# Kernel optimization log

Hardware: AMD Instinct MI355X
Metric: run time of the kernel (lower is better)

The kernel has to match this reference:

```python
import jax, jax.numpy as jnp
import numpy as np

EPS = 1e-08
F_DIM = 512


def setup_inputs() -> dict:
    key = jax.random.key(0)
    ks = jax.random.split(key, 7)
    N, F = 50000, F_DIM
    q = jax.random.normal(ks[0], (N, 1, F), dtype=jnp.float32)
    mu = jax.random.normal(ks[1], (N, 3, F), dtype=jnp.float32)
    # Xavier-ish scaled params
    W_mix = jax.random.normal(ks[2], (2 * F, F), dtype=jnp.float32) * (1.0 / np.sqrt(F))
    W1 = jax.random.normal(ks[3], (F, 2 * F), dtype=jnp.float32) * (1.0 / np.sqrt(2 * F))
    b1 = jnp.zeros((F,), dtype=jnp.float32)
    W2 = jax.random.normal(ks[4], (3 * F, F), dtype=jnp.float32) * (1.0 / np.sqrt(F))
    b2 = jnp.zeros((3 * F,), dtype=jnp.float32)
    return {"q": q, "mu": mu, "W_mix": W_mix, "W1": W1, "b1": b1, "W2": W2, "b2": b2}


def reference(q, mu, W_mix, W1, b1, W2, b2):
    F = q.shape[-1]
    # mu_channel_mix: [N,3,F] @ [F,2F] -> [N,3,2F]
    mu_mix = jnp.einsum('ndf,gf->ndg', mu, W_mix)
    mu_V, mu_W = mu_mix[..., :F], mu_mix[..., F:]
    # vector norm over Cartesian axis -> [N,1,F]
    mu_Vn = jnp.sqrt(jnp.sum(mu_V * mu_V, axis=-2, keepdims=True) + EPS)
    ctx = jnp.concatenate([q, mu_Vn], axis=-1)  # [N,1,2F]
    h = jax.nn.silu(jnp.einsum('nsf,gf->nsg', ctx, W1) + b1)  # [N,1,F]
    x = jnp.einsum('nsf,gf->nsg', h, W2) + b2  # [N,1,3F]
    dq_intra = x[..., :F]
    dmu_intra = x[..., F:2 * F] * mu_W  # broadcast [N,1,F]*[N,3,F]
    dqmu_intra = x[..., 2 * F:] * jnp.sum(mu_V * mu_W, axis=1, keepdims=True)
    q_out = q + dq_intra + dqmu_intra
    mu_out = mu + dmu_intra
    return (q_out, mu_out)
```

## Files before the change

kernel.cpp:

```cpp
#include <hip/hip_runtime.h>
#include <stdint.h>

#define NN 50000
#define QWORDS 25600000

typedef __attribute__((ext_vector_type(8))) short bf16x8;
typedef __attribute__((ext_vector_type(4))) float f32x4;

__device__ __forceinline__ uint32_t f2bf(float x){
  uint32_t u = __builtin_bit_cast(uint32_t, x);
  u += 0x7FFFu + ((u >> 16) & 1u);
  return u >> 16;
}
__device__ __forceinline__ float bf2f(uint32_t b){
  uint32_t u = b << 16;
  return __builtin_bit_cast(float, u);
}
__device__ __forceinline__ void gload16(const uint16_t* g, uint16_t* l){
  __builtin_amdgcn_global_load_lds(
      (const __attribute__((address_space(1))) uint32_t*)g,
      (__attribute__((address_space(3))) uint32_t*)l, 16, 0, 0);
}
__device__ __forceinline__ f32x4 mfma16(bf16x8 a, bf16x8 b, f32x4 c){
  return __builtin_amdgcn_mfma_f32_16x16x32_bf16(a, b, c, 0, 0, 0);
}

#define FENCE() asm volatile("" ::: "memory")

__global__ void k_convert(const float* __restrict__ wmix, const float* __restrict__ w1,
                          const float* __restrict__ w2, uint16_t* __restrict__ dst){
  int i = blockIdx.x * 256 + threadIdx.x;
  int e = i << 2;
  const float* s; int o;
  if (e < 524288)       { s = wmix; o = e; }
  else if (e < 1048576) { s = w1;   o = e - 524288; }
  else                  { s = w2;   o = e - 1048576; }
  f32x4 v = *(const f32x4*)(s + o);
  uint2 pk;
  pk.x = f2bf(v[0]) | (f2bf(v[1]) << 16);
  pk.y = f2bf(v[2]) | (f2bf(v[3]) << 16);
  *(uint2*)(dst + e) = pk;
}

__global__ __launch_bounds__(512, 4)
void k_gemm1(const float* __restrict__ mu, const uint16_t* __restrict__ wmixb,
             uint16_t* __restrict__ qh, float* __restrict__ muW){
  __shared__ uint16_t As[2][12288];
  __shared__ uint16_t Bs[2][8192];
  const int tid  = threadIdx.x;
  const int lane = tid & 63;
  const int w    = tid >> 6;
  const int wn   = w & 3;
  const int wf   = w >> 2;
  const int orig = blockIdx.x;
  const int j    = (orig & 7) * 782 + (orig >> 3);
  const int f0   = (j & 7) * 64;
  const int n0   = (j >> 3) * 64;
  const int lrow = tid >> 4;
  const int lcol = (tid & 15) * 4;

  f32x4 ar[6];
  auto A_LOAD = [&](int ks){
    const int k0 = ks * 64;
    #pragma unroll
    for (int p=0; p<6; ++p){
      int r = p*32 + lrow;
      int d = r >> 6, nrow = r & 63;
      int n = n0 + nrow;
      int g = (n < NN ? n : NN-1)*3 + d;
      ar[p] = *(const f32x4*)(mu + (size_t)g*512 + k0 + lcol);
    }
  };
  auto A_WRITE = [&](int buf){
    #pragma unroll
    for (int p=0; p<6; ++p){
      int r = p*32 + lrow;
      f32x4 v = ar[p];
      uint2 pk;
      pk.x = f2bf(v[0]) | (f2bf(v[1]) << 16);
      pk.y = f2bf(v[2]) | (f2bf(v[3]) << 16);
      *(uint2*)&As[buf][r*64 + (lcol ^ ((r&7)<<3))] = pk;
    }
  };
  auto B_ISSUE = [&](int ks, int buf){
    const int k0 = ks * 64;
    #pragma unroll
    for (int jj=0; jj<2; ++jj){
      int jb = w*2 + jj;
      int row = jb*8 + (lane>>3);
      int g = (row < 64) ? (f0 + row) : (448 + f0 + row);
      int srcc = ((lane&7) ^ ((lane>>3)&7)) * 8;
      gload16(wmixb + (size_t)g*512 + k0 + srcc, &Bs[buf][jb*512]);
    }
  };

  const f32x4 z4 = {0.f,0.f,0.f,0.f};
  f32x4 acc[3][4];
  #pragma unroll
  for (int d=0; d<3; ++d)
    #pragma unroll
    for (int nt=0; nt<4; ++nt) acc[d][nt] = z4;

  A_LOAD(0); B_ISSUE(0, 0); A_WRITE(0);
  for (int ks=0; ks<8; ++ks){
    const int cur = ks & 1;
    __syncthreads();
    if (ks < 7){ A_LOAD(ks+1); B_ISSUE(ks+1, cur^1); }
    #pragma unroll
    for (int kf=0; kf<2; ++kf){
      int kc = kf*32 + (lane>>4)*8;
      bf16x8 af[3];
      #pragma unroll
      for (int d=0; d<3; ++d){
        int r = d*64 + wn*16 + (lane&15);
        af[d] = *(const bf16x8*)&As[cur][r*64 + (kc ^ ((r&7)<<3))];
      }
      #pragma unroll
      for (int nt=0; nt<4; ++nt){
        int ntg = wf*2 + (nt&1) + (nt>>1)*4;
        int rr = ntg*16 + (lane&15);
        bf16x8 bf = *(const bf16x8*)&Bs[cur][rr*64 + (kc ^ ((rr&7)<<3))];
        #pragma unroll
        for (int d=0; d<3; ++d)
          acc[d][nt] = mfma16(af[d], bf, acc[d][nt]);
      }
    }
    if (ks < 7) A_WRITE(cur^1);
  }

  const int rb4 = (lane >> 4) * 4;
  #pragma unroll
  for (int c=0; c<2; ++c){
    #pragma unroll
    for (int jx=0; jx<4; ++jx){
      int n = n0 + wn*16 + rb4 + jx;
      if (n >= NN) continue;
      int f = f0 + (wf*2 + c)*16 + (lane & 15);
      float v0 = acc[0][c][jx],   v1 = acc[1][c][jx],   v2 = acc[2][c][jx];
      float u0 = acc[0][c+2][jx], u1 = acc[1][c+2][jx], u2 = acc[2][c+2][jx];
      float vn = sqrtf(v0*v0 + v1*v1 + v2*v2 + 1e-8f);
      float dt = v0*u0 + v1*u1 + v2*u2;
      qh[(size_t)n*1024 + f]       = (uint16_t)f2bf(vn);
      qh[(size_t)n*1024 + 512 + f] = (uint16_t)f2bf(dt);
      size_t mb = (size_t)n*1536 + f;
      muW[mb] = u0; muW[mb+512] = u1; muW[mb+1024] = u2;
    }
  }
}

__global__ __launch_bounds__(256, 2)
void k_gemm2(const float* __restrict__ q, const uint16_t* __restrict__ w1b,
             const float* __restrict__ b1, uint16_t* __restrict__ qh){
  __shared__ uint16_t A2[2][2048];
  __shared__ uint16_t B2[2][16384];
  const int tid  = threadIdx.x;
  const int lane = tid & 63;
  const int w    = tid >> 6;
  const int wm   = w >> 1;
  const int wn   = w & 1;
  const int n0   = blockIdx.x * 64;

  f32x4 qa0, qa1;
  auto QA_LOAD = [&](int s){
    int k0 = s*32;
    int row = tid >> 2, ch = tid & 3;
    int nc = (n0 + row < NN) ? n0 + row : NN-1;
    qa0 = *(const f32x4*)(q + (size_t)nc*512 + k0 + ch*8);
    qa1 = *(const f32x4*)(q + (size_t)nc*512 + k0 + ch*8 + 4);
  };
  auto QA_WRITE = [&](int buf){
    int row = tid >> 2, ch = tid & 3;
    uint4 pk;
    pk.x = f2bf(qa0[0]) | (f2bf(qa0[1]) << 16);
    pk.y = f2bf(qa0[2]) | (f2bf(qa0[3]) << 16);
    pk.z = f2bf(qa1[0]) | (f2bf(qa1[1]) << 16);
    pk.w = f2bf(qa1[2]) | (f2bf(qa1[3]) << 16);
    *(uint4*)&A2[buf][row*32 + ((ch ^ (row&3)))*8] = pk;
  };
  auto VA_ISSUE = [&](int s, int buf){
    int k0v = (s-16)*32;
    int row = w*16 + (lane>>2);
    int nc = (n0 + row < NN) ? n0 + row : NN-1;
    int srcch = (lane&3) ^ (row&3);
    gload16(qh + (size_t)nc*1024 + k0v + srcch*8, &A2[buf][w*512]);
  };
  auto B_ISSUE = [&](int s, int buf){
    int k0 = s*32;
    #pragma unroll
    for (int jj=0; jj<8; ++jj){
      int j = w*8 + jj;
      int row = j*16 + (lane>>2);
      int srcch = (lane&3) ^ (row&3);
      gload16(w1b + (size_t)row*1024 + k0 + srcch*8, &B2[buf][j*512]);
    }
  };

  const f32x4 z4 = {0.f,0.f,0.f,0.f};
  f32x4 acc2[2][16];
  #pragma unroll
  for (int mt=0; mt<2; ++mt)
    #pragma unroll
    for (int nt=0; nt<16; ++nt) acc2[mt][nt] = z4;

  QA_LOAD(0); B_ISSUE(0, 0); QA_WRITE(0);
  for (int s=0; s<32; ++s){
    const int cur = s & 1;
    __syncthreads();
    if (s < 31){
      if (s+1 < 16) QA_LOAD(s+1); else VA_ISSUE(s+1, cur^1);
      B_ISSUE(s+1, cur^1);
    }
    {
      int kc = (lane>>4)*8;
      bf16x8 a[2];
      #pragma unroll
      for (int mt=0; mt<2; ++mt){
        int r = wm*32 + mt*16 + (lane&15);
        a[mt] = *(const bf16x8*)&A2[cur][r*32 + (kc ^ ((r&3)<<3))];
      }
      #pragma unroll
      for (int nt=0; nt<16; ++nt){
        int rr = wn*256 + nt*16 + (lane&15);
        bf16x8 b = *(const bf16x8*)&B2[cur][rr*32 + (kc ^ ((rr&3)<<3))];
        acc2[0][nt] = mfma16(a[0], b, acc2[0][nt]);
        acc2[1][nt] = mfma16(a[1], b, acc2[1][nt]);
      }
    }
    if (s < 31 && s+1 < 16) QA_WRITE(cur^1);
  }

  const int rb4 = (lane >> 4) * 4;
  #pragma unroll
  for (int nt=0; nt<16; ++nt){
    int col = wn*256 + nt*16 + (lane&15);
    float bb = b1[col];
    #pragma unroll
    for (int mt=0; mt<2; ++mt)
      #pragma unroll
      for (int j=0; j<4; ++j){
        int n = n0 + wm*32 + mt*16 + rb4 + j;
        if (n < NN){
          float x = acc2[mt][nt][j] + bb;
          float sv = x / (1.f + __expf(-x));
          qh[(size_t)n*1024 + col] = (uint16_t)f2bf(sv);
        }
      }
  }
}

__global__ __launch_bounds__(512, 4)
void k_gemm3(const float* __restrict__ q, const float* __restrict__ mu,
             const uint16_t* __restrict__ w2b, const float* __restrict__ b2,
             float* __restrict__ dout){
  __shared__ uint16_t Hs[32*512];
  __shared__ uint16_t B3[2][12288];
  const int tid  = threadIdx.x;
  const int lane = tid & 63;
  const int w    = tid >> 6;
  const int wm   = w >> 2;
  const int wn   = w & 3;
  const int n0   = blockIdx.x * 32;
  const uint16_t* qh = (const uint16_t*)dout;
  float* mout = dout + (size_t)QWORDS;
  const int l15 = lane & 15;
  const int rb4 = (lane >> 4) * 4;
  const f32x4 z4 = {0.f,0.f,0.f,0.f};

  #pragma unroll
  for (int i=0; i<4; ++i){
    int row = w*4 + i;
    int nc = (n0 + row < NN) ? n0 + row : NN-1;
    gload16(qh + (size_t)nc*1024 + (size_t)((lane ^ (row&7))*8), &Hs[row*512]);
  }

  auto B_ISSUE = [&](int it, int ks, uint16_t* slot){
    #pragma unroll
    for (int jj=0; jj<3; ++jj){
      int j = w*3 + jj;
      int rr = j*8 + (lane>>3);
      int s3 = rr >> 6, fi = rr & 63;
      int g = s3*512 + it*64 + fi;
      gload16(w2b + (size_t)g*512 + ks*64 + ((lane&7) ^ (rr&7))*8, slot + j*512);
    }
  };
  B_ISSUE(0, 0, B3[0]);

  float dtv[4], qv[4], muv[3][4], mwv[3][4];
  float bb0=0.f, bb1=0.f, bb2=0.f;
  int   fq = 0;
  f32x4 acc3[3];

#define K3_MFMA(KS) do{ \
    const uint16_t* bsl = B3[(KS)&1]; \
    __builtin_amdgcn_s_setprio(1); \
    _Pragma("unroll") \
    for (int kf=0; kf<2; ++kf){ \
      int r = wm*16 + l15; \
      int ch = ((KS)*8 + kf*4 + (lane>>4)) ^ (r&7); \
      bf16x8 a = *(const bf16x8*)&Hs[r*512 + ch*8]; \
      _Pragma("unroll") \
      for (int s3=0; s3<3; ++s3){ \
        int rr = s3*64 + wn*16 + l15; \
        int chb = (kf*4 + (lane>>4)) ^ (rr&7); \
        bf16x8 b = *(const bf16x8*)&bsl[rr*64 + chb*8]; \
        acc3[s3] = mfma16(a, b, acc3[s3]); \
      } \
    } \
    __builtin_amdgcn_s_setprio(0); \
  } while(0)

  #pragma unroll 1
  for (int it=0; it<8; ++it){
    if (it) { asm volatile("s_waitcnt vmcnt(16)" ::: "memory"); }
    else    { asm volatile("s_waitcnt vmcnt(0)"  ::: "memory"); }
    __builtin_amdgcn_s_barrier();
    B_ISSUE(it, 1, B3[1]);
    FENCE();
    {
      #pragma unroll
      for (int s3=0; s3<3; ++s3) acc3[s3] = z4;
      fq = it*64 + wn*16 + l15;
      bb0 = b2[fq]; bb1 = b2[512+fq]; bb2 = b2[1024+fq];
      #pragma unroll
      for (int p=0; p<4; ++p){
        int n = n0 + wm*16 + rb4 + p;
        int nc = n < NN ? n : NN-1;
        dtv[p] = bf2f(qh[(size_t)nc*1024 + 512 + fq]);
        qv[p]  = q[(size_t)nc*512 + fq];
      }
    }
    FENCE();
    K3_MFMA(0);

    asm volatile("s_waitcnt vmcnt(11)" ::: "memory");
    __builtin_amdgcn_s_barrier();
    B_ISSUE(it, 2, B3[0]);
    FENCE();
    {
      #pragma unroll
      for (int p=0; p<4; ++p){
        int n = n0 + wm*16 + rb4 + p;
        int nc = n < NN ? n : NN-1;
        size_t mb = (size_t)nc*1536 + fq;
        muv[0][p] = mu[mb]; muv[1][p] = mu[mb+512]; muv[2][p] = mu[mb+1024];
      }
    }
    FENCE();
    K3_MFMA(1);

    asm volatile("s_waitcnt vmcnt(12)" ::: "memory");
    __builtin_amdgcn_s_barrier();
    B_ISSUE(it, 3, B3[1]);
    FENCE();
    {
      #pragma unroll
      for (int p=0; p<4; ++p){
        int n = n0 + wm*16 + rb4 + p;
        int nc = n < NN ? n : NN-1;
        size_t mb = (size_t)nc*1536 + fq;
        mwv[0][p] = mout[mb]; mwv[1][p] = mout[mb+512]; mwv[2][p] = mout[mb+1024];
      }
    }
    FENCE();
    K3_MFMA(2);

    asm volatile("s_waitcnt vmcnt(12)" ::: "memory");
    __builtin_amdgcn_s_barrier();
    B_ISSUE(it, 4, B3[0]);
    FENCE();
    K3_MFMA(3);

    asm volatile("s_waitcnt vmcnt(0)" ::: "memory");
    __builtin_amdgcn_s_barrier();
    B_ISSUE(it, 5, B3[1]);
    FENCE();
    K3_MFMA(4);

    asm volatile("s_waitcnt vmcnt(0)" ::: "memory");
    __builtin_amdgcn_s_barrier();
    B_ISSUE(it, 6, B3[0]);
    FENCE();
    K3_MFMA(5);

    asm volatile("s_waitcnt vmcnt(0)" ::: "memory");
    __builtin_amdgcn_s_barrier();
    B_ISSUE(it, 7, B3[1]);
    FENCE();
    K3_MFMA(6);

    asm volatile("s_waitcnt vmcnt(0)" ::: "memory");
    __builtin_amdgcn_s_barrier();
    if (it < 7) B_ISSUE(it+1, 0, B3[0]);
    FENCE();
    K3_MFMA(7);
    {
      #pragma unroll
      for (int p=0; p<4; ++p){
        int n = n0 + wm*16 + rb4 + p;
        if (n < NN){
          float x0 = acc3[0][p] + bb0;
          float x1 = acc3[1][p] + bb1;
          float x2 = acc3[2][p] + bb2;
          dout[(size_t)n*512 + fq] = qv[p] + x0 + x2*dtv[p];
          size_t mb = (size_t)n*1536 + fq;
          mout[mb]      = muv[0][p] + x1*mwv[0][p];
          mout[mb+512]  = muv[1][p] + x1*mwv[1][p];
          mout[mb+1024] = muv[2][p] + x1*mwv[2][p];
        }
      }
    }
  }
#undef K3_MFMA
}

extern "C" void kernel_launch(void* const* d_in, const int* in_sizes, int n_in,
                              void* d_out, int out_size, void* d_ws, size_t ws_size,
                              hipStream_t stream){
  (void)in_sizes; (void)n_in; (void)out_size; (void)ws_size;
  const float* q    = (const float*)d_in[0];
  const float* mu   = (const float*)d_in[1];
  const float* wmix = (const float*)d_in[2];
  const float* w1   = (const float*)d_in[3];
  const float* b1   = (const float*)d_in[4];
  const float* w2   = (const float*)d_in[5];
  const float* b2   = (const float*)d_in[6];
  uint16_t* wb = (uint16_t*)d_ws;
  float* dout = (float*)d_out;

  hipLaunchKernelGGL(k_convert, dim3(1792), dim3(256), 0, stream, wmix, w1, w2, wb);
  hipLaunchKernelGGL(k_gemm1, dim3(6256), dim3(512), 0, stream,
                     mu, wb, (uint16_t*)d_out, dout + (size_t)QWORDS);
  hipLaunchKernelGGL(k_gemm2, dim3(782), dim3(256), 0, stream,
                     q, wb + 524288, b1, (uint16_t*)d_out);
  hipLaunchKernelGGL(k_gemm3, dim3(1563), dim3(512), 0, stream,
                     q, mu, wb + 1048576, b2, dout);
}
```

Measured before the change: 895.2 us.

## Load W2 fragments directly into registers and stage full hidden row in LDS

New measurement: 1.361 ms. 52.0% more time.

```diff
diff --git a/kernel.cpp b/kernel.cpp
--- a/kernel.cpp
+++ b/kernel.cpp
@@ -24,8 +24,6 @@
 __device__ __forceinline__ f32x4 mfma16(bf16x8 a, bf16x8 b, f32x4 c){
   return __builtin_amdgcn_mfma_f32_16x16x32_bf16(a, b, c, 0, 0, 0);
 }
-
-#define FENCE() asm volatile("" ::: "memory")
 
 __global__ void k_convert(const float* __restrict__ wmix, const float* __restrict__ w1,
                           const float* __restrict__ w2, uint16_t* __restrict__ dst){
@@ -252,8 +250,7 @@
 void k_gemm3(const float* __restrict__ q, const float* __restrict__ mu,
              const uint16_t* __restrict__ w2b, const float* __restrict__ b2,
              float* __restrict__ dout){
-  __shared__ uint16_t Hs[32*512];
-  __shared__ uint16_t B3[2][12288];
+  __shared__ uint16_t Hs[32*1024];
   const int tid  = threadIdx.x;
   const int lane = tid & 63;
   const int w    = tid >> 6;
@@ -264,153 +261,86 @@
   float* mout = dout + (size_t)QWORDS;
   const int l15 = lane & 15;
   const int rb4 = (lane >> 4) * 4;
-  const f32x4 z4 = {0.f,0.f,0.f,0.f};
+  const int kof = (lane >> 4) * 8;
 
   #pragma unroll
   for (int i=0; i<4; ++i){
     int row = w*4 + i;
     int nc = (n0 + row < NN) ? n0 + row : NN-1;
-    gload16(qh + (size_t)nc*1024 + (size_t)((lane ^ (row&7))*8), &Hs[row*512]);
-  }
-
-  auto B_ISSUE = [&](int it, int ks, uint16_t* slot){
-    #pragma unroll
-    for (int jj=0; jj<3; ++jj){
-      int j = w*3 + jj;
-      int rr = j*8 + (lane>>3);
-      int s3 = rr >> 6, fi = rr & 63;
-      int g = s3*512 + it*64 + fi;
-      gload16(w2b + (size_t)g*512 + ks*64 + ((lane&7) ^ (rr&7))*8, slot + j*512);
-    }
-  };
-  B_ISSUE(0, 0, B3[0]);
-
-  float dtv[4], qv[4], muv[3][4], mwv[3][4];
-  float bb0=0.f, bb1=0.f, bb2=0.f;
-  int   fq = 0;
-  f32x4 acc3[3];
-
-#define K3_MFMA(KS) do{ \
-    const uint16_t* bsl = B3[(KS)&1]; \
-    __builtin_amdgcn_s_setprio(1); \
-    _Pragma("unroll") \
-    for (int kf=0; kf<2; ++kf){ \
-      int r = wm*16 + l15; \
-      int ch = ((KS)*8 + kf*4 + (lane>>4)) ^ (r&7); \
-      bf16x8 a = *(const bf16x8*)&Hs[r*512 + ch*8]; \
-      _Pragma("unroll") \
-      for (int s3=0; s3<3; ++s3){ \
-        int rr = s3*64 + wn*16 + l15; \
-        int chb = (kf*4 + (lane>>4)) ^ (rr&7); \
-        bf16x8 b = *(const bf16x8*)&bsl[rr*64 + chb*8]; \
-        acc3[s3] = mfma16(a, b, acc3[s3]); \
-      } \
-    } \
-    __builtin_amdgcn_s_setprio(0); \
-  } while(0)
+    int sc = (lane ^ (row&7)) * 8;
+    gload16(qh + (size_t)nc*1024 + sc,       &Hs[row*1024]);
+    gload16(qh + (size_t)nc*1024 + 512 + sc, &Hs[row*1024 + 512]);
+  }
+  asm volatile("s_waitcnt vmcnt(0)" ::: "memory");
+  __syncthreads();
+
+  int nidx[4], rowp[4];
+  #pragma unroll
+  for (int p=0; p<4; ++p){
+    int rr = wm*16 + rb4 + p;
+    rowp[p] = rr;
+    int n = n0 + rr;
+    nidx[p] = n < NN ? n : NN-1;
+  }
 
   #pragma unroll 1
   for (int it=0; it<8; ++it){
-    if (it) { asm volatile("s_waitcnt vmcnt(16)" ::: "memory"); }
-    else    { asm volatile("s_waitcnt vmcnt(0)"  ::: "memory"); }
-    __builtin_amdgcn_s_barrier();
-    B_ISSUE(it, 1, B3[1]);
-    FENCE();
-    {
-      #pragma unroll
-      for (int s3=0; s3<3; ++s3) acc3[s3] = z4;
-      fq = it*64 + wn*16 + l15;
-      bb0 = b2[fq]; bb1 = b2[512+fq]; bb2 = b2[1024+fq];
-      #pragma unroll
-      for (int p=0; p<4; ++p){
-        int n = n0 + wm*16 + rb4 + p;
-        int nc = n < NN ? n : NN-1;
-        dtv[p] = bf2f(qh[(size_t)nc*1024 + 512 + fq]);
-        qv[p]  = q[(size_t)nc*512 + fq];
-      }
-    }
-    FENCE();
-    K3_MFMA(0);
-
-    asm volatile("s_waitcnt vmcnt(11)" ::: "memory");
-    __builtin_amdgcn_s_barrier();
-    B_ISSUE(it, 2, B3[0]);
-    FENCE();
-    {
-      #pragma unroll
-      for (int p=0; p<4; ++p){
-        int n = n0 + wm*16 + rb4 + p;
-        int nc = n < NN ? n : NN-1;
-        size_t mb = (size_t)nc*1536 + fq;
-        muv[0][p] = mu[mb]; muv[1][p] = mu[mb+512]; muv[2][p] = mu[mb+1024];
-      }
-    }
-    FENCE();
-    K3_MFMA(1);
-
-    asm volatile("s_waitcnt vmcnt(12)" ::: "memory");
-    __builtin_amdgcn_s_barrier();
-    B_ISSUE(it, 3, B3[1]);
-    FENCE();
-    {
-      #pragma unroll
-      for (int p=0; p<4; ++p){
-        int n = n0 + wm*16 + rb4 + p;
-        int nc = n < NN ? n : NN-1;
-        size_t mb = (size_t)nc*1536 + fq;
-        mwv[0][p] = mout[mb]; mwv[1][p] = mout[mb+512]; mwv[2][p] = mout[mb+1024];
-      }
-    }
-    FENCE();
-    K3_MFMA(2);
-
-    asm volatile("s_waitcnt vmcnt(12)" ::: "memory");
-    __builtin_amdgcn_s_barrier();
-    B_ISSUE(it, 4, B3[0]);
-    FENCE();
-    K3_MFMA(3);
-
-    asm volatile("s_waitcnt vmcnt(0)" ::: "memory");
-    __builtin_amdgcn_s_barrier();
-    B_ISSUE(it, 5, B3[1]);
-    FENCE();
-    K3_MFMA(4);
-
-    asm volatile("s_waitcnt vmcnt(0)" ::: "memory");
-    __builtin_amdgcn_s_barrier();
-    B_ISSUE(it, 6, B3[0]);
-    FENCE();
-    K3_MFMA(5);
-
-    asm volatile("s_waitcnt vmcnt(0)" ::: "memory");
-    __builtin_amdgcn_s_barrier();
-    B_ISSUE(it, 7, B3[1]);
-    FENCE();
-    K3_MFMA(6);
-
-    asm volatile("s_waitcnt vmcnt(0)" ::: "memory");
-    __builtin_amdgcn_s_barrier();
-    if (it < 7) B_ISSUE(it+1, 0, B3[0]);
-    FENCE();
-    K3_MFMA(7);
-    {
-      #pragma unroll
-      for (int p=0; p<4; ++p){
-        int n = n0 + wm*16 + rb4 + p;
-        if (n < NN){
-          float x0 = acc3[0][p] + bb0;
-          float x1 = acc3[1][p] + bb1;
-          float x2 = acc3[2][p] + bb2;
-          dout[(size_t)n*512 + fq] = qv[p] + x0 + x2*dtv[p];
-          size_t mb = (size_t)n*1536 + fq;
-          mout[mb]      = muv[0][p] + x1*mwv[0][p];
-          mout[mb+512]  = muv[1][p] + x1*mwv[1][p];
-          mout[mb+1024] = muv[2][p] + x1*mwv[2][p];
-        }
-      }
-    }
-  }
-#undef K3_MFMA
+    const int fq = it*64 + wn*16 + l15;
+    const float bb0 = b2[fq], bb1 = b2[512+fq], bb2 = b2[1024+fq];
+    float qv[4], dtv[4], muv[3][4], mwv[3][4];
+    const int dc = fq >> 3, dо = fq & 7;
+    #pragma unroll
+    for (int p=0; p<4; ++p){
+      dtv[p] = bf2f(Hs[rowp[p]*1024 + 512 + ((dc ^ (rowp[p]&7))*8) + dо]);
+      qv[p]  = q[(size_t)nidx[p]*512 + fq];
+      size_t mb = (size_t)nidx[p]*1536 + fq;
+      muv[0][p] = mu[mb];   muv[1][p] = mu[mb+512];   muv[2][p] = mu[mb+1024];
+      mwv[0][p] = mout[mb]; mwv[1][p] = mout[mb+512]; mwv[2][p] = mout[mb+1024];
+    }
+
+    f32x4 acc0 = {0.f,0.f,0.f,0.f}, acc1 = acc0, acc2 = acc0;
+    const uint16_t* bp0 = w2b + (size_t)(it*64 + wn*16 + l15)*512;
+    bf16x8 bc[6], bn[6];
+    auto LDB = [&](bf16x8* dst, int ks){
+      const int ko = ks*64 + kof;
+      #pragma unroll
+      for (int s3=0; s3<3; ++s3){
+        const uint16_t* bp = bp0 + (size_t)s3*512*512;
+        dst[s3*2+0] = *(const bf16x8*)(bp + ko);
+        dst[s3*2+1] = *(const bf16x8*)(bp + ko + 32);
+      }
+    };
+    LDB(bc, 0);
+    #pragma unroll
+    for (int ks=0; ks<8; ++ks){
+      if (ks < 7) LDB(bn, ks+1);
+      const int r = wm*16 + l15;
+      const int ch0 = (ks*8 + 0 + (lane>>4)) ^ (r&7);
+      const int ch1 = (ks*8 + 4 + (lane>>4)) ^ (r&7);
+      bf16x8 a0 = *(const bf16x8*)&Hs[r*1024 + ch0*8];
+      bf16x8 a1 = *(const bf16x8*)&Hs[r*1024 + ch1*8];
+      acc0 = mfma16(a0, bc[0], acc0); acc0 = mfma16(a1, bc[1], acc0);
+      acc1 = mfma16(a0, bc[2], acc1); acc1 = mfma16(a1, bc[3], acc1);
+      acc2 = mfma16(a0, bc[4], acc2); acc2 = mfma16(a1, bc[5], acc2);
+      #pragma unroll
+      for (int z=0; z<6; ++z) bc[z] = bn[z];
+    }
+
+    #pragma unroll
+    for (int p=0; p<4; ++p){
+      int n = n0 + wm*16 + rb4 + p;
+      if (n < NN){
+        float x0 = acc0[p] + bb0;
+        float x1 = acc1[p] + bb1;
+        float x2 = acc2[p] + bb2;
+        dout[(size_t)n*512 + fq] = qv[p] + x0 + x2*dtv[p];
+        size_t mb = (size_t)n*1536 + fq;
+        mout[mb]      = muv[0][p] + x1*mwv[0][p];
+        mout[mb+512]  = muv[1][p] + x1*mwv[1][p];
+        mout[mb+1024] = muv[2][p] + x1*mwv[2][p];
+      }
+    }
+  }
 }
 
 extern "C" void kernel_launch(void* const* d_in, const int* in_sizes, int n_in,
```
